# Kernel optimization log

Hardware: AMD Instinct MI355X
Metric: run time of the kernel (lower is better)

The kernel has to match this reference:

```python
import jax, jax.numpy as jnp
import numpy as np

H = 128  # GRU hidden size

def gru_cell(x, h, Wih, Whh, bih, bhh):
    # torch GRU gate order: r, z, n
    gx = x @ Wih.T + bih          # (B, 3H)
    gh = h @ Whh.T + bhh          # (B, 3H)
    xr, xz, xn = jnp.split(gx, 3, axis=-1)
    hr, hz, hn = jnp.split(gh, 3, axis=-1)
    r = jax.nn.sigmoid(xr + hr)
    z = jax.nn.sigmoid(xz + hz)
    n = jnp.tanh(xn + r * hn)
    return (1.0 - z) * n + z * h

def conv2d(x, w, b, stride):
    y = jax.lax.conv_general_dilated(x, w, window_strides=(stride, stride), padding='VALID',
                                     dimension_numbers=('NCHW', 'OIHW', 'NCHW'))
    return y + b[None, :, None, None]

def setup_inputs() -> dict:
    key = jax.random.key(0)
    ks = jax.random.split(key, 20)
    B, T = 8192, 64
    s = lambda *sh: 0.1
    inp = {
        'cnn_states': jax.random.normal(ks[0], (B, 8, 8, 27), jnp.float32),
        'linears_states': jax.random.normal(ks[1], (B, T, 29), jnp.float32),
        'conv1_w': jax.random.normal(ks[2], (16, 27, 3, 3), jnp.float32) * 0.1,
        'conv1_b': jnp.zeros((16,), jnp.float32),
        'conv2_w': jax.random.normal(ks[3], (32, 16, 2, 2), jnp.float32) * 0.1,
        'conv2_b': jnp.zeros((32,), jnp.float32),
        'fc_w': jax.random.normal(ks[4], (128, 128), jnp.float32) * 0.1,
        'fc_b': jnp.zeros((128,), jnp.float32),
        'enc_Wih': jax.random.normal(ks[5], (3 * H, 29), jnp.float32) * 0.1,
        'enc_Whh': jax.random.normal(ks[6], (3 * H, H), jnp.float32) * 0.1,
        'enc_bih': jnp.zeros((3 * H,), jnp.float32),
        'enc_bhh': jnp.zeros((3 * H,), jnp.float32),
        'dec_Wih': jax.random.normal(ks[7], (3 * H, H), jnp.float32) * 0.1,
        'dec_Whh': jax.random.normal(ks[8], (3 * H, H), jnp.float32) * 0.1,
        'dec_bih': jnp.zeros((3 * H,), jnp.float32),
        'dec_bhh': jnp.zeros((3 * H,), jnp.float32),
        'dis_w': jax.random.normal(ks[9], (78, 256), jnp.float32) * 0.01,
        'dis_b': jnp.zeros((78,), jnp.float32),
        'value_w': jax.random.normal(ks[10], (1, 256), jnp.float32) * 0.1,
        'value_b': jnp.zeros((1,), jnp.float32),
    }
    return inp

def _forward(cnn_states, linears_states, conv1_w, conv1_b, conv2_w, conv2_b, fc_w, fc_b,
             enc_Wih, enc_Whh, enc_bih, enc_bhh, dec_Wih, dec_Whh, dec_bih, dec_bhh,
             dis_w, dis_b, value_w, value_b):
    B, T = linears_states.shape[0], linears_states.shape[1]
    # CNN encoder (NHWC -> NCHW)
    x = jnp.transpose(cnn_states, (0, 3, 1, 2))
    x = jax.nn.relu(conv2d(x, conv1_w, conv1_b, 2))   # (B,16,3,3)
    x = jax.nn.relu(conv2d(x, conv2_w, conv2_b, 1))   # (B,32,2,2)
    x = x.reshape(B, -1)                               # (B,128), CHW order matches torch Flatten
    z_cnn = jax.nn.relu(x @ fc_w.T + fc_b)             # (B,128)

    # encoder GRU over linears_states
    xs = jnp.transpose(linears_states, (1, 0, 2))      # (T,B,29)
    h0 = jnp.zeros((B, H), linears_states.dtype)
    def enc_step(h, xt):
        h2 = gru_cell(xt, h, enc_Wih, enc_Whh, enc_bih, enc_bhh)
        return h2, None
    h_enc, _ = jax.lax.scan(enc_step, h0, xs)

    x0 = jnp.zeros((B, H), linears_states.dtype)
    def dec_step(carry, _):
        xin, h = carry
        h2 = gru_cell(xin, h, dec_Wih, dec_Whh, dec_bih, dec_bhh)
        return (h2, h2), None
    (z_pn, _), _ = jax.lax.scan(dec_step, (x0, h_enc), None, length=T)

    pn = jnp.concatenate([z_cnn, z_pn], axis=1)        # (B,256)
    distris = pn @ dis_w.T + dis_b                     # (B,78)
    value = pn @ value_w.T + value_b                   # (B,1)
    return distris, value

def reference(cnn_states, linears_states, conv1_w, conv1_b, conv2_w, conv2_b, fc_w, fc_b,
              enc_Wih, enc_Whh, enc_bih, enc_bhh, dec_Wih, dec_Whh, dec_bih, dec_bhh,
              dis_w, dis_b, value_w, value_b):
    return _forward(cnn_states, linears_states, conv1_w, conv1_b, conv2_w, conv2_b, fc_w, fc_b,
                    enc_Wih, enc_Whh, enc_bih, enc_bhh, dec_Wih, dec_Whh, dec_bih, dec_bhh,
                    dis_w, dis_b, value_w, value_b)
```

## Files before the change

kernel.cpp:

```cpp
#include <hip/hip_runtime.h>

typedef _Float16 f16;
typedef _Float16 f16x8 __attribute__((ext_vector_type(8)));
typedef float f32x4 __attribute__((ext_vector_type(4)));

#define WS_ZCNN 0
#define WS_EWIH 4194304
#define WS_EWHH 4218880
#define WS_DWC  4317184
#define WS_DWHH 4448256
#define WS_BIAS 4546560
#define WS_W1F  4550656
#define WS_W2F  4559872
#define WS_FCWF 4563968

static __device__ __forceinline__ f32x4 mfma16(f16x8 a, f16x8 b, f32x4 c) {
    return __builtin_amdgcn_mfma_f32_16x16x32_f16(a, b, c, 0, 0, 0);
}
static __device__ __forceinline__ float fexp2n(float x) {
    return __builtin_amdgcn_exp2f(x * -1.4426950408889634f);
}

__global__ void k_prep(const float* __restrict__ eWih, const float* __restrict__ eWhh,
                       const float* __restrict__ ebih, const float* __restrict__ ebhh,
                       const float* __restrict__ dWih, const float* __restrict__ dWhh,
                       const float* __restrict__ dbih, const float* __restrict__ dbhh,
                       const float* __restrict__ w1, const float* __restrict__ w2,
                       const float* __restrict__ fcw,
                       char* __restrict__ ws)
{
    f16* ewih = (f16*)(ws + WS_EWIH);
    f16* ewhh = (f16*)(ws + WS_EWHH);
    f16* dwc  = (f16*)(ws + WS_DWC);
    f16* dwhh = (f16*)(ws + WS_DWHH);
    float* bias = (float*)(ws + WS_BIAS);
    f16* w1f = (f16*)(ws + WS_W1F);
    f16* w2f = (f16*)(ws + WS_W2F);
    f16* fcwf = (f16*)(ws + WS_FCWF);
    const int total = 12288 + 49152 + 65536 + 49152 + 1024 + 4608 + 2048 + 16384;
    for (int i = blockIdx.x * 256 + threadIdx.x; i < total; i += gridDim.x * 256) {
        int j = i;
        if (j < 12288) { int g = j >> 5, k = j & 31;
            ewih[j] = (f16)((k < 29) ? eWih[g * 29 + k] : 0.0f); continue; }
        j -= 12288;
        if (j < 49152) { ewhh[j] = (f16)eWhh[j]; continue; }
        j -= 49152;
        if (j < 65536) { int row = j >> 7, k = j & 127; float v;
            if (row < 256)      v = dWih[row * 128 + k] + dWhh[row * 128 + k];
            else if (row < 384) v = dWih[row * 128 + k];
            else                v = dWhh[(row - 128) * 128 + k];
            dwc[j] = (f16)v; continue; }
        j -= 65536;
        if (j < 49152) { dwhh[j] = (f16)dWhh[j]; continue; }
        j -= 49152;
        if (j < 1024) {
            if (j < 256)        bias[j] = ebih[j] + ebhh[j];
            else if (j < 384)   bias[j] = ebih[j];
            else if (j < 512)   bias[j] = ebhh[j - 128];
            else if (j < 768)   bias[j] = dbih[j - 512] + dbhh[j - 512];
            else if (j < 896)   bias[j] = dbih[j - 512];
            else                bias[j] = dbhh[j - 640];
            continue; }
        j -= 1024;
        if (j < 4608) {
            int kk = j >> 9, rem = j & 511, co = rem >> 5, k = rem & 31;
            w1f[j] = (f16)((k < 27) ? w1[co * 243 + k * 9 + kk] : 0.0f); continue; }
        j -= 4608;
        if (j < 2048) {
            int s = j >> 10, rem = j & 1023, co = rem >> 5, k = rem & 31;
            int kk2 = 2 * s + (k >= 16), ci = k & 15;
            w2f[j] = (f16)w2[co * 64 + ci * 4 + kk2]; continue; }
        j -= 2048;
        fcwf[j] = (f16)fcw[j];
    }
}

__global__ __launch_bounds__(256) void k_cnn(
    const float* __restrict__ cin,
    const float* __restrict__ b1, const float* __restrict__ b2,
    const float* __restrict__ fcb,
    char* __restrict__ ws)
{
    __shared__ __align__(16) f16 in_t[16][64][32];
    __shared__ __align__(16) f16 a1f[16][9][24];
    __shared__ __align__(16) f16 vf[16][136];

    const int tid = threadIdx.x;
    const int base = blockIdx.x * 16;
    const f16* w1f = (const f16*)(ws + WS_W1F);
    const f16* w2f = (const f16*)(ws + WS_W2F);
    const f16* fcwf = (const f16*)(ws + WS_FCWF);
    float* z = (float*)(ws + WS_ZCNN);

    for (int i = tid; i < 16 * 1728; i += 256) {
        int img = i / 1728, rem = i % 1728;
        int pix = rem / 27, ci = rem % 27;
        in_t[img][pix][ci] = (f16)cin[(size_t)base * 1728 + i];
    }
    for (int i = tid; i < 16 * 64 * 5; i += 256) {
        int img = i / 320, r2 = i % 320;
        in_t[img][r2 / 5][27 + r2 % 5] = (f16)0.0f;
    }
    __syncthreads();

    const int wv = tid >> 6, lane = tid & 63, nl = lane & 15, quad = lane >> 4;

    f16x8 bw1[9];
    #pragma unroll
    for (int kk = 0; kk < 9; kk++)
        bw1[kk] = *(const f16x8*)(w1f + (kk * 16 + nl) * 32 + quad * 8);
    float b1v = b1[nl];
    for (int p = wv; p < 9; p += 4) {
        int oy = p / 3, ox = p % 3;
        f32x4 acc = {b1v, b1v, b1v, b1v};
        #pragma unroll
        for (int kk = 0; kk < 9; kk++) {
            int pix = (2 * oy + kk / 3) * 8 + (2 * ox + kk % 3);
            f16x8 a = *(const f16x8*)(&in_t[nl][pix][quad * 8]);
            acc = mfma16(a, bw1[kk], acc);
        }
        #pragma unroll
        for (int r = 0; r < 4; r++)
            a1f[quad * 4 + r][p][nl] = (f16)fmaxf(acc[r], 0.0f);
    }
    __syncthreads();

    {
        int y = wv >> 1, x = wv & 1;
        #pragma unroll
        for (int nt = 0; nt < 2; nt++) {
            float bv = b2[nt * 16 + nl];
            f32x4 acc = {bv, bv, bv, bv};
            #pragma unroll
            for (int s = 0; s < 2; s++) {
                int kk2 = 2 * s + (quad >> 1);
                int pos1 = (y + (kk2 >> 1)) * 3 + (x + (kk2 & 1));
                f16x8 a = *(const f16x8*)(&a1f[nl][pos1][(quad & 1) * 8]);
                f16x8 b = *(const f16x8*)(w2f + ((size_t)s * 32 + nt * 16 + nl) * 32 + quad * 8);
                acc = mfma16(a, b, acc);
            }
            #pragma unroll
            for (int r = 0; r < 4; r++)
                vf[quad * 4 + r][(nt * 16 + nl) * 4 + (y * 2 + x)] = (f16)fmaxf(acc[r], 0.0f);
        }
    }
    __syncthreads();

    #pragma unroll
    for (int nt = 0; nt < 2; nt++) {
        int o = wv * 32 + nt * 16 + nl;
        float bv = fcb[o];
        f32x4 acc = {bv, bv, bv, bv};
        #pragma unroll
        for (int kt = 0; kt < 4; kt++) {
            f16x8 a = *(const f16x8*)(&vf[nl][kt * 32 + quad * 8]);
            f16x8 b = *(const f16x8*)(fcwf + o * 128 + kt * 32 + quad * 8);
            acc = mfma16(a, b, acc);
        }
        #pragma unroll
        for (int r = 0; r < 4; r++)
            z[(size_t)(base + quad * 4 + r) * 128 + o] = fmaxf(acc[r], 0.0f);
    }
}

__global__ __launch_bounds__(512, 4) void k_gru(
    const float* __restrict__ lin,
    const char* __restrict__ ws,
    const float* __restrict__ dis_w, const float* __restrict__ dis_b,
    const float* __restrict__ value_w, const float* __restrict__ value_b,
    float* __restrict__ out)
{
    const int tid = threadIdx.x;
    const int wv = tid >> 6;
    const int lane = tid & 63;
    const int nl = lane & 15;
    const int quad = lane >> 4;
    const int j0 = wv * 16;
    const int row0 = blockIdx.x * 16;

    const f16* ewih = (const f16*)(ws + WS_EWIH);
    const f16* ewhh = (const f16*)(ws + WS_EWHH);
    const f16* dwc  = (const f16*)(ws + WS_DWC);
    const f16* dwhh = (const f16*)(ws + WS_DWHH);
    const float* bias = (const float*)(ws + WS_BIAS);
    const float* z_cnn = (const float*)(ws + WS_ZCNN);

    __shared__ __align__(16) f16 h_s[2][16][136];
    __shared__ __align__(16) f16 x_s[2][16][32];
    __shared__ __align__(16) float pn_s[16][264];

    for (int i = tid; i < 2 * 16 * 136; i += 512) ((f16*)h_s)[i] = (f16)0.0f;

    const int rsw = (nl & 8) ? 16 : 0;
    const int wrow = quad * 4;
    const int wsw = (quad >= 2) ? 16 : 0;
    const int wcol = (j0 + nl + wsw) & 127;

    float ho[4];
    #pragma unroll
    for (int r = 0; r < 4; r++) ho[r] = 0.0f;

    const int xr = tid >> 5, xc = tid & 31;

    {
        float eb_r, eb_z, eb_xn, eb_hn;
        { int c = j0 + nl;
          eb_r = bias[c]; eb_z = bias[128 + c]; eb_xn = bias[256 + c]; eb_hn = bias[384 + c]; }
        f16x8 we_r[4], we_z[4], we_hn[4], we_xr, we_xz, we_xn;
        { int gr = j0 + nl;
          #pragma unroll
          for (int kt = 0; kt < 4; kt++) {
              we_r[kt]  = *(const f16x8*)(ewhh + gr * 128 + kt * 32 + quad * 8);
              we_z[kt]  = *(const f16x8*)(ewhh + (128 + gr) * 128 + kt * 32 + quad * 8);
              we_hn[kt] = *(const f16x8*)(ewhh + (256 + gr) * 128 + kt * 32 + quad * 8);
          }
          we_xr = *(const f16x8*)(ewih + gr * 32 + quad * 8);
          we_xz = *(const f16x8*)(ewih + (128 + gr) * 32 + quad * 8);
          we_xn = *(const f16x8*)(ewih + (256 + gr) * 32 + quad * 8);
        }

        float xv = (xc < 29) ? lin[(size_t)(row0 + xr) * 1856 + xc] : 0.0f;

        for (int t = 0; t < 64; t++) {
            x_s[t & 1][xr][xc] = (f16)xv;
            __syncthreads();
            f16x8 ax = *(const f16x8*)(&x_s[t & 1][nl][quad * 8]);
            f16x8 ah[4];
            #pragma unroll
            for (int kt = 0; kt < 4; kt++)
                ah[kt] = *(const f16x8*)(&h_s[t & 1][nl][((kt * 32 + quad * 8 + rsw) & 127)]);
            if (t < 63) xv = (xc < 29) ? lin[(size_t)(row0 + xr) * 1856 + (t + 1) * 29 + xc] : 0.0f;

            f32x4 aR  = {eb_r, eb_r, eb_r, eb_r};
            f32x4 aZ  = {eb_z, eb_z, eb_z, eb_z};
            f32x4 aXN = {eb_xn, eb_xn, eb_xn, eb_xn};
            f32x4 aHN = {eb_hn, eb_hn, eb_hn, eb_hn};
            aR  = mfma16(ax, we_xr, aR);
            aZ  = mfma16(ax, we_xz, aZ);
            aXN = mfma16(ax, we_xn, aXN);
            #pragma unroll
            for (int kt = 0; kt < 4; kt++) {
                aR  = mfma16(ah[kt], we_r[kt], aR);
                aZ  = mfma16(ah[kt], we_z[kt], aZ);
                aHN = mfma16(ah[kt], we_hn[kt], aHN);
            }
            #pragma unroll
            for (int r = 0; r < 4; r++) {
                float ea = fexp2n(aR[r]), eb = fexp2n(aZ[r]);
                float s1 = 1.0f + ea, s2 = 1.0f + eb;
                float R = __builtin_amdgcn_rcpf(s1 * s2);
                float rg = s2 * R, zg = s1 * R;
                float ec = fexp2n(2.0f * (aXN[r] + rg * aHN[r]));
                float ng = (1.0f - ec) * __builtin_amdgcn_rcpf(1.0f + ec);
                float h = (1.0f - zg) * ng + zg * ho[r];
                ho[r] = h;
                h_s[(t + 1) & 1][wrow + r][wcol] = (f16)h;
            }
        }
    }

    float db_r, db_z, db_xn, db_hn;
    { int c = j0 + nl;
      db_r = bias[512 + c]; db_z = bias[640 + c]; db_xn = bias[768 + c]; db_hn = bias[896 + c]; }

    {
        __syncthreads();
        f16x8 ah[4];
        #pragma unroll
        for (int kt = 0; kt < 4; kt++)
            ah[kt] = *(const f16x8*)(&h_s[0][nl][((kt * 32 + quad * 8 + rsw) & 127)]);
        int gr = j0 + nl;
        f32x4 aR  = {db_r, db_r, db_r, db_r};
        f32x4 aZ  = {db_z, db_z, db_z, db_z};
        f32x4 aHN = {db_hn, db_hn, db_hn, db_hn};
        #pragma unroll
        for (int kt = 0; kt < 4; kt++) {
            aR  = mfma16(ah[kt], *(const f16x8*)(dwhh + gr * 128 + kt * 32 + quad * 8), aR);
            aZ  = mfma16(ah[kt], *(const f16x8*)(dwhh + (128 + gr) * 128 + kt * 32 + quad * 8), aZ);
            aHN = mfma16(ah[kt], *(const f16x8*)(dwhh + (256 + gr) * 128 + kt * 32 + quad * 8), aHN);
        }
        #pragma unroll
        for (int r = 0; r < 4; r++) {
            float ea = fexp2n(aR[r]), eb = fexp2n(aZ[r]);
            float s1 = 1.0f + ea, s2 = 1.0f + eb;
            float R = __builtin_amdgcn_rcpf(s1 * s2);
            float rg = s2 * R, zg = s1 * R;
            float ec = fexp2n(2.0f * (db_xn + rg * aHN[r]));
            float ng = (1.0f - ec) * __builtin_amdgcn_rcpf(1.0f + ec);
            float h = (1.0f - zg) * ng + zg * ho[r];
            ho[r] = h;
            h_s[1][wrow + r][wcol] = (f16)h;
        }
    }
    {
        f16x8 wd_r[4], wd_z[4], wd_xn[4], wd_hn[4];
        { int gr = j0 + nl;
          #pragma unroll
          for (int kt = 0; kt < 4; kt++) {
              wd_r[kt]  = *(const f16x8*)(dwc + gr * 128 + kt * 32 + quad * 8);
              wd_z[kt]  = *(const f16x8*)(dwc + (128 + gr) * 128 + kt * 32 + quad * 8);
              wd_xn[kt] = *(const f16x8*)(dwc + (256 + gr) * 128 + kt * 32 + quad * 8);
              wd_hn[kt] = *(const f16x8*)(dwc + (384 + gr) * 128 + kt * 32 + quad * 8);
          }
        }
        for (int t = 1; t < 64; t++) {
            __syncthreads();
            f16x8 ah[4];
            #pragma unroll
            for (int kt = 0; kt < 4; kt++)
                ah[kt] = *(const f16x8*)(&h_s[t & 1][nl][((kt * 32 + quad * 8 + rsw) & 127)]);
            f32x4 aR  = {db_r, db_r, db_r, db_r};
            f32x4 aZ  = {db_z, db_z, db_z, db_z};
            f32x4 aXN = {db_xn, db_xn, db_xn, db_xn};
            f32x4 aHN = {db_hn, db_hn, db_hn, db_hn};
            #pragma unroll
            for (int kt = 0; kt < 4; kt++) {
                aR  = mfma16(ah[kt], wd_r[kt], aR);
                aZ  = mfma16(ah[kt], wd_z[kt], aZ);
                aXN = mfma16(ah[kt], wd_xn[kt], aXN);
                aHN = mfma16(ah[kt], wd_hn[kt], aHN);
            }
            #pragma unroll
            for (int r = 0; r < 4; r++) {
                float ea = fexp2n(aR[r]), eb = fexp2n(aZ[r]);
                float s1 = 1.0f + ea, s2 = 1.0f + eb;
                float R = __builtin_amdgcn_rcpf(s1 * s2);
                float rg = s2 * R, zg = s1 * R;
                float ec = fexp2n(2.0f * (aXN[r] + rg * aHN[r]));
                float ng = (1.0f - ec) * __builtin_amdgcn_rcpf(1.0f + ec);
                float h = (1.0f - zg) * ng + zg * ho[r];
                ho[r] = h;
                h_s[(t + 1) & 1][wrow + r][wcol] = (f16)h;
            }
        }
    }

    #pragma unroll
    for (int r = 0; r < 4; r++)
        pn_s[wrow + r][128 + j0 + nl] = ho[r];
    for (int i = tid; i < 16 * 128; i += 512) {
        int rr = i >> 7, cc = i & 127;
        pn_s[rr][cc] = z_cnn[(size_t)(row0 + rr) * 128 + cc];
    }
    __syncthreads();

    const int rr = tid & 15, og = tid >> 4;
    const float4* pr4 = (const float4*)(&pn_s[rr][0]);
    for (int o = og; o < 79; o += 32) {
        const float* wrow_p = (o < 78) ? (dis_w + o * 256) : value_w;
        float acc = (o < 78) ? dis_b[o] : value_b[0];
        const float4* wr4 = (const float4*)wrow_p;
        #pragma unroll 8
        for (int k = 0; k < 64; k++) {
            float4 a = wr4[k], b = pr4[k];
            acc += a.x * b.x + a.y * b.y + a.z * b.z + a.w * b.w;
        }
        if (o < 78) out[(size_t)(row0 + rr) * 78 + o] = acc;
        else        out[(size_t)8192 * 78 + row0 + rr] = acc;
    }
}

extern "C" void kernel_launch(void* const* d_in, const int* in_sizes, int n_in,
                              void* d_out, int out_size, void* d_ws, size_t ws_size,
                              hipStream_t stream)
{
    (void)in_sizes; (void)n_in; (void)out_size; (void)ws_size;
    const float* cnn  = (const float*)d_in[0];
    const float* lin  = (const float*)d_in[1];
    const float* c1w  = (const float*)d_in[2];
    const float* c1b  = (const float*)d_in[3];
    const float* c2w  = (const float*)d_in[4];
    const float* c2b  = (const float*)d_in[5];
    const float* fcw  = (const float*)d_in[6];
    const float* fcb  = (const float*)d_in[7];
    const float* eWih = (const float*)d_in[8];
    const float* eWhh = (const float*)d_in[9];
    const float* ebih = (const float*)d_in[10];
    const float* ebhh = (const float*)d_in[11];
    const float* dWih = (const float*)d_in[12];
    const float* dWhh = (const float*)d_in[13];
    const float* dbih = (const float*)d_in[14];
    const float* dbhh = (const float*)d_in[15];
    const float* disw = (const float*)d_in[16];
    const float* disb = (const float*)d_in[17];
    const float* vw   = (const float*)d_in[18];
    const float* vb   = (const float*)d_in[19];
    char* ws = (char*)d_ws;
    float* out = (float*)d_out;

    hipLaunchKernelGGL(k_prep, dim3(128), dim3(256), 0, stream,
                       eWih, eWhh, ebih, ebhh, dWih, dWhh, dbih, dbhh,
                       c1w, c2w, fcw, ws);
    hipLaunchKernelGGL(k_cnn, dim3(512), dim3(256), 0, stream,
                       cnn, c1b, c2b, fcb, ws);
    hipLaunchKernelGGL(k_gru, dim3(512), dim3(512), 0, stream,
                       lin, ws, disw, disb, vw, vb, out);
}
```

Baseline: 380.9 us.

## Unroll GRU loops by two, relax launch bounds, and pad CNN input stride

The encoder and decoder recurrences are unrolled by two with constant double-buffer indices, and the h_s column offsets are hoisted into precomputed constants. The k_gru launch bound's minimum blocks per CU drops from 4 to 2, giving the compiler more registers per thread at the cost of possibly fewer resident waves. The k_cnn input tile gets a padded per-image stride of 2088 halves instead of 2048, aimed at reducing LDS bank conflicts on the MFMA A-operand loads. Together these are meant to remove spills and per-step indexing overhead on the latency-bound recurrent loop.

```diff
diff --git a/kernel.cpp b/kernel.cpp
--- a/kernel.cpp
+++ b/kernel.cpp
@@ -75,13 +75,14 @@
     }
 }
 
+#define IMG_STRIDE 2088
 __global__ __launch_bounds__(256) void k_cnn(
     const float* __restrict__ cin,
     const float* __restrict__ b1, const float* __restrict__ b2,
     const float* __restrict__ fcb,
     char* __restrict__ ws)
 {
-    __shared__ __align__(16) f16 in_t[16][64][32];
+    __shared__ __align__(16) f16 in_f[16 * IMG_STRIDE];
     __shared__ __align__(16) f16 a1f[16][9][24];
     __shared__ __align__(16) f16 vf[16][136];
 
@@ -95,11 +96,11 @@
     for (int i = tid; i < 16 * 1728; i += 256) {
         int img = i / 1728, rem = i % 1728;
         int pix = rem / 27, ci = rem % 27;
-        in_t[img][pix][ci] = (f16)cin[(size_t)base * 1728 + i];
+        in_f[img * IMG_STRIDE + pix * 32 + ci] = (f16)cin[(size_t)base * 1728 + i];
     }
     for (int i = tid; i < 16 * 64 * 5; i += 256) {
         int img = i / 320, r2 = i % 320;
-        in_t[img][r2 / 5][27 + r2 % 5] = (f16)0.0f;
+        in_f[img * IMG_STRIDE + (r2 / 5) * 32 + 27 + r2 % 5] = (f16)0.0f;
     }
     __syncthreads();
 
@@ -116,7 +117,7 @@
         #pragma unroll
         for (int kk = 0; kk < 9; kk++) {
             int pix = (2 * oy + kk / 3) * 8 + (2 * ox + kk % 3);
-            f16x8 a = *(const f16x8*)(&in_t[nl][pix][quad * 8]);
+            f16x8 a = *(const f16x8*)(&in_f[nl * IMG_STRIDE + pix * 32 + quad * 8]);
             acc = mfma16(a, bw1[kk], acc);
         }
         #pragma unroll
@@ -163,7 +164,7 @@
     }
 }
 
-__global__ __launch_bounds__(512, 4) void k_gru(
+__global__ __launch_bounds__(512, 2) void k_gru(
     const float* __restrict__ lin,
     const char* __restrict__ ws,
     const float* __restrict__ dis_w, const float* __restrict__ dis_b,
@@ -195,12 +196,18 @@
     const int wrow = quad * 4;
     const int wsw = (quad >= 2) ? 16 : 0;
     const int wcol = (j0 + nl + wsw) & 127;
+    const int c0 = (quad * 8 + rsw) & 127;
+    const int c1 = (32 + quad * 8 + rsw) & 127;
+    const int c2 = (64 + quad * 8 + rsw) & 127;
+    const int c3 = (96 + quad * 8 + rsw) & 127;
 
     float ho[4];
     #pragma unroll
     for (int r = 0; r < 4; r++) ho[r] = 0.0f;
 
     const int xr = tid >> 5, xc = tid & 31;
+    const bool xok = (xc < 29);
+    const size_t lin_base = (size_t)(row0 + xr) * 1856 + xc;
 
     {
         float eb_r, eb_z, eb_xn, eb_hn;
@@ -219,44 +226,50 @@
           we_xn = *(const f16x8*)(ewih + (256 + gr) * 32 + quad * 8);
         }
 
-        float xv = (xc < 29) ? lin[(size_t)(row0 + xr) * 1856 + xc] : 0.0f;
-
-        for (int t = 0; t < 64; t++) {
-            x_s[t & 1][xr][xc] = (f16)xv;
-            __syncthreads();
-            f16x8 ax = *(const f16x8*)(&x_s[t & 1][nl][quad * 8]);
-            f16x8 ah[4];
-            #pragma unroll
-            for (int kt = 0; kt < 4; kt++)
-                ah[kt] = *(const f16x8*)(&h_s[t & 1][nl][((kt * 32 + quad * 8 + rsw) & 127)]);
-            if (t < 63) xv = (xc < 29) ? lin[(size_t)(row0 + xr) * 1856 + (t + 1) * 29 + xc] : 0.0f;
-
-            f32x4 aR  = {eb_r, eb_r, eb_r, eb_r};
-            f32x4 aZ  = {eb_z, eb_z, eb_z, eb_z};
-            f32x4 aXN = {eb_xn, eb_xn, eb_xn, eb_xn};
-            f32x4 aHN = {eb_hn, eb_hn, eb_hn, eb_hn};
-            aR  = mfma16(ax, we_xr, aR);
-            aZ  = mfma16(ax, we_xz, aZ);
-            aXN = mfma16(ax, we_xn, aXN);
-            #pragma unroll
-            for (int kt = 0; kt < 4; kt++) {
-                aR  = mfma16(ah[kt], we_r[kt], aR);
-                aZ  = mfma16(ah[kt], we_z[kt], aZ);
-                aHN = mfma16(ah[kt], we_hn[kt], aHN);
-            }
-            #pragma unroll
-            for (int r = 0; r < 4; r++) {
-                float ea = fexp2n(aR[r]), eb = fexp2n(aZ[r]);
-                float s1 = 1.0f + ea, s2 = 1.0f + eb;
-                float R = __builtin_amdgcn_rcpf(s1 * s2);
-                float rg = s2 * R, zg = s1 * R;
-                float ec = fexp2n(2.0f * (aXN[r] + rg * aHN[r]));
-                float ng = (1.0f - ec) * __builtin_amdgcn_rcpf(1.0f + ec);
-                float h = (1.0f - zg) * ng + zg * ho[r];
-                ho[r] = h;
-                h_s[(t + 1) & 1][wrow + r][wcol] = (f16)h;
-            }
-        }
+        float xv = xok ? lin[lin_base] : 0.0f;
+
+#define ENC_STEP(BUF, OBUF, TN)                                                      \
+        do {                                                                         \
+            x_s[BUF][xr][xc] = (f16)xv;                                              \
+            __syncthreads();                                                         \
+            f16x8 ax = *(const f16x8*)(&x_s[BUF][nl][quad * 8]);                     \
+            f16x8 ah0 = *(const f16x8*)(&h_s[BUF][nl][c0]);                          \
+            f16x8 ah1 = *(const f16x8*)(&h_s[BUF][nl][c1]);                          \
+            f16x8 ah2 = *(const f16x8*)(&h_s[BUF][nl][c2]);                          \
+            f16x8 ah3 = *(const f16x8*)(&h_s[BUF][nl][c3]);                          \
+            if ((TN) < 64) xv = xok ? lin[lin_base + (TN) * 29] : 0.0f;              \
+            f32x4 aR  = {eb_r, eb_r, eb_r, eb_r};                                    \
+            f32x4 aZ  = {eb_z, eb_z, eb_z, eb_z};                                    \
+            f32x4 aXN = {eb_xn, eb_xn, eb_xn, eb_xn};                                \
+            f32x4 aHN = {eb_hn, eb_hn, eb_hn, eb_hn};                                \
+            aR  = mfma16(ax, we_xr, aR);                                             \
+            aZ  = mfma16(ax, we_xz, aZ);                                             \
+            aXN = mfma16(ax, we_xn, aXN);                                            \
+            aR  = mfma16(ah0, we_r[0], aR);  aR  = mfma16(ah1, we_r[1], aR);         \
+            aR  = mfma16(ah2, we_r[2], aR);  aR  = mfma16(ah3, we_r[3], aR);         \
+            aZ  = mfma16(ah0, we_z[0], aZ);  aZ  = mfma16(ah1, we_z[1], aZ);         \
+            aZ  = mfma16(ah2, we_z[2], aZ);  aZ  = mfma16(ah3, we_z[3], aZ);         \
+            aHN = mfma16(ah0, we_hn[0], aHN); aHN = mfma16(ah1, we_hn[1], aHN);      \
+            aHN = mfma16(ah2, we_hn[2], aHN); aHN = mfma16(ah3, we_hn[3], aHN);      \
+            _Pragma("unroll")                                                        \
+            for (int r = 0; r < 4; r++) {                                            \
+                float ea = fexp2n(aR[r]), eb = fexp2n(aZ[r]);                        \
+                float s1 = 1.0f + ea, s2 = 1.0f + eb;                                \
+                float R = __builtin_amdgcn_rcpf(s1 * s2);                            \
+                float rg = s2 * R, zg = s1 * R;                                      \
+                float ec = fexp2n(2.0f * (aXN[r] + rg * aHN[r]));                    \
+                float ng = (1.0f - ec) * __builtin_amdgcn_rcpf(1.0f + ec);           \
+                float h = (1.0f - zg) * ng + zg * ho[r];                             \
+                ho[r] = h;                                                           \
+                h_s[OBUF][wrow + r][wcol] = (f16)h;                                  \
+            }                                                                        \
+        } while (0)
+
+        for (int t = 0; t < 64; t += 2) {
+            ENC_STEP(0, 1, t + 1);
+            ENC_STEP(1, 0, t + 2);
+        }
+#undef ENC_STEP
     }
 
     float db_r, db_z, db_xn, db_hn;
@@ -265,19 +278,23 @@
 
     {
         __syncthreads();
-        f16x8 ah[4];
-        #pragma unroll
-        for (int kt = 0; kt < 4; kt++)
-            ah[kt] = *(const f16x8*)(&h_s[0][nl][((kt * 32 + quad * 8 + rsw) & 127)]);
+        f16x8 ah0 = *(const f16x8*)(&h_s[0][nl][c0]);
+        f16x8 ah1 = *(const f16x8*)(&h_s[0][nl][c1]);
+        f16x8 ah2 = *(const f16x8*)(&h_s[0][nl][c2]);
+        f16x8 ah3 = *(const f16x8*)(&h_s[0][nl][c3]);
         int gr = j0 + nl;
         f32x4 aR  = {db_r, db_r, db_r, db_r};
         f32x4 aZ  = {db_z, db_z, db_z, db_z};
         f32x4 aHN = {db_hn, db_hn, db_hn, db_hn};
         #pragma unroll
         for (int kt = 0; kt < 4; kt++) {
-            aR  = mfma16(ah[kt], *(const f16x8*)(dwhh + gr * 128 + kt * 32 + quad * 8), aR);
-            aZ  = mfma16(ah[kt], *(const f16x8*)(dwhh + (128 + gr) * 128 + kt * 32 + quad * 8), aZ);
-            aHN = mfma16(ah[kt], *(const f16x8*)(dwhh + (256 + gr) * 128 + kt * 32 + quad * 8), aHN);
+            f16x8 b0 = *(const f16x8*)(dwhh + gr * 128 + kt * 32 + quad * 8);
+            f16x8 b1 = *(const f16x8*)(dwhh + (128 + gr) * 128 + kt * 32 + quad * 8);
+            f16x8 b2 = *(const f16x8*)(dwhh + (256 + gr) * 128 + kt * 32 + quad * 8);
+            f16x8 a = (kt == 0) ? ah0 : (kt == 1) ? ah1 : (kt == 2) ? ah2 : ah3;
+            aR  = mfma16(a, b0, aR);
+            aZ  = mfma16(a, b1, aZ);
+            aHN = mfma16(a, b2, aHN);
         }
         #pragma unroll
         for (int r = 0; r < 4; r++) {
@@ -303,36 +320,46 @@
               wd_hn[kt] = *(const f16x8*)(dwc + (384 + gr) * 128 + kt * 32 + quad * 8);
           }
         }
-        for (int t = 1; t < 64; t++) {
-            __syncthreads();
-            f16x8 ah[4];
-            #pragma unroll
-            for (int kt = 0; kt < 4; kt++)
-                ah[kt] = *(const f16x8*)(&h_s[t & 1][nl][((kt * 32 + quad * 8 + rsw) & 127)]);
-            f32x4 aR  = {db_r, db_r, db_r, db_r};
-            f32x4 aZ  = {db_z, db_z, db_z, db_z};
-            f32x4 aXN = {db_xn, db_xn, db_xn, db_xn};
-            f32x4 aHN = {db_hn, db_hn, db_hn, db_hn};
-            #pragma unroll
-            for (int kt = 0; kt < 4; kt++) {
-                aR  = mfma16(ah[kt], wd_r[kt], aR);
-                aZ  = mfma16(ah[kt], wd_z[kt], aZ);
-                aXN = mfma16(ah[kt], wd_xn[kt], aXN);
-                aHN = mfma16(ah[kt], wd_hn[kt], aHN);
-            }
-            #pragma unroll
-            for (int r = 0; r < 4; r++) {
-                float ea = fexp2n(aR[r]), eb = fexp2n(aZ[r]);
-                float s1 = 1.0f + ea, s2 = 1.0f + eb;
-                float R = __builtin_amdgcn_rcpf(s1 * s2);
-                float rg = s2 * R, zg = s1 * R;
-                float ec = fexp2n(2.0f * (aXN[r] + rg * aHN[r]));
-                float ng = (1.0f - ec) * __builtin_amdgcn_rcpf(1.0f + ec);
-                float h = (1.0f - zg) * ng + zg * ho[r];
-                ho[r] = h;
-                h_s[(t + 1) & 1][wrow + r][wcol] = (f16)h;
-            }
-        }
+
+#define DEC_STEP(BUF, OBUF)                                                          \
+        do {                                                                         \
+            __syncthreads();                                                         \
+            f16x8 ah0 = *(const f16x8*)(&h_s[BUF][nl][c0]);                          \
+            f16x8 ah1 = *(const f16x8*)(&h_s[BUF][nl][c1]);                          \
+            f16x8 ah2 = *(const f16x8*)(&h_s[BUF][nl][c2]);                          \
+            f16x8 ah3 = *(const f16x8*)(&h_s[BUF][nl][c3]);                          \
+            f32x4 aR  = {db_r, db_r, db_r, db_r};                                    \
+            f32x4 aZ  = {db_z, db_z, db_z, db_z};                                    \
+            f32x4 aXN = {db_xn, db_xn, db_xn, db_xn};                                \
+            f32x4 aHN = {db_hn, db_hn, db_hn, db_hn};                                \
+            aR  = mfma16(ah0, wd_r[0], aR);   aR  = mfma16(ah1, wd_r[1], aR);        \
+            aR  = mfma16(ah2, wd_r[2], aR);   aR  = mfma16(ah3, wd_r[3], aR);        \
+            aZ  = mfma16(ah0, wd_z[0], aZ);   aZ  = mfma16(ah1, wd_z[1], aZ);        \
+            aZ  = mfma16(ah2, wd_z[2], aZ);   aZ  = mfma16(ah3, wd_z[3], aZ);        \
+            aXN = mfma16(ah0, wd_xn[0], aXN); aXN = mfma16(ah1, wd_xn[1], aXN);      \
+            aXN = mfma16(ah2, wd_xn[2], aXN); aXN = mfma16(ah3, wd_xn[3], aXN);      \
+            aHN = mfma16(ah0, wd_hn[0], aHN); aHN = mfma16(ah1, wd_hn[1], aHN);      \
+            aHN = mfma16(ah2, wd_hn[2], aHN); aHN = mfma16(ah3, wd_hn[3], aHN);      \
+            _Pragma("unroll")                                                        \
+            for (int r = 0; r < 4; r++) {                                            \
+                float ea = fexp2n(aR[r]), eb = fexp2n(aZ[r]);                        \
+                float s1 = 1.0f + ea, s2 = 1.0f + eb;                                \
+                float R = __builtin_amdgcn_rcpf(s1 * s2);                            \
+                float rg = s2 * R, zg = s1 * R;                                      \
+                float ec = fexp2n(2.0f * (aXN[r] + rg * aHN[r]));                    \
+                float ng = (1.0f - ec) * __builtin_amdgcn_rcpf(1.0f + ec);           \
+                float h = (1.0f - zg) * ng + zg * ho[r];                             \
+                ho[r] = h;                                                           \
+                h_s[OBUF][wrow + r][wcol] = (f16)h;                                  \
+            }                                                                        \
+        } while (0)
+
+        DEC_STEP(1, 0);
+        for (int t = 2; t < 64; t += 2) {
+            DEC_STEP(0, 1);
+            DEC_STEP(1, 0);
+        }
+#undef DEC_STEP
     }
 
     #pragma unroll
```

After: 396.6 us. +4.1%, slower.
